# Kernel optimization log

Measured on AMD Instinct MI355X. Metric: run time of the kernel, lower is better.

The kernel has to match this reference:

```python
import jax, jax.numpy as jnp
from jax import lax
import numpy as np

RADIUS = 0.3
NSAMPLES = 32
SPATIAL_STRIDE = 32
TKS = 3
TSTRIDE = 2
DIM = 512
DEPTH = 4
HEADS = 8
DIM_HEAD = 64
MLP_DIM = 1024
NUM_CLASSES = 30
B, T, N = 4, 24, 4096


def setup_inputs():
    key = jax.random.key(0)
    ks = jax.random.split(key, 16)
    def w(k, shape, fan_in):
        return jax.random.normal(k, shape, jnp.float32) / np.float32(np.sqrt(fan_in))
    return {
        "xyzs": jax.random.uniform(ks[0], (B, T, N, 3), jnp.float32),
        "old_features": jax.random.normal(ks[1], (B, T, 2, N), jnp.float32),
        "conv_d_w": w(ks[2], (DIM, 4), 4),
        "conv_f_w": w(ks[3], (DIM, 2), 2),
        "pos_w": w(ks[4], (DIM, 4), 4),
        "pos_b": jnp.zeros((DIM,), jnp.float32),
        "contr_w": w(ks[5], (DIM, 4), 4),
        "contr_b": jnp.zeros((DIM,), jnp.float32),
        "ln1_s": jnp.ones((DEPTH, DIM), jnp.float32),
        "ln1_b": jnp.zeros((DEPTH, DIM), jnp.float32),
        "qkv_w": w(ks[6], (DEPTH, 3 * HEADS * DIM_HEAD, DIM), DIM),
        "out_w": w(ks[7], (DEPTH, DIM, HEADS * DIM_HEAD), HEADS * DIM_HEAD),
        "out_b": jnp.zeros((DEPTH, DIM), jnp.float32),
        "ln2_s": jnp.ones((DEPTH, DIM), jnp.float32),
        "ln2_b": jnp.zeros((DEPTH, DIM), jnp.float32),
        "ff1_w": w(ks[8], (DEPTH, MLP_DIM, DIM), DIM),
        "ff1_b": jnp.zeros((DEPTH, MLP_DIM), jnp.float32),
        "ff2_w": w(ks[9], (DEPTH, DIM, MLP_DIM), MLP_DIM),
        "ff2_b": jnp.zeros((DEPTH, DIM), jnp.float32),
        "head_ln_s": jnp.ones((DIM,), jnp.float32),
        "head_ln_b": jnp.zeros((DIM,), jnp.float32),
        "head1_w": w(ks[10], (MLP_DIM, DIM), DIM),
        "head1_b": jnp.zeros((MLP_DIM,), jnp.float32),
        "head2_w": w(ks[11], (NUM_CLASSES, MLP_DIM), MLP_DIM),
        "head2_b": jnp.zeros((NUM_CLASSES,), jnp.float32),
    }


def _fps(xyz, npoint):
    # furthest point sampling, pointnet2 semantics (start at index 0)
    n = xyz.shape[0]
    def body(carry, _):
        dist, last = carry
        d = jnp.sum((xyz - xyz[last]) ** 2, axis=-1)
        dist = jnp.minimum(dist, d)
        nxt = jnp.argmax(dist).astype(jnp.int32)
        return (dist, nxt), nxt
    init = (jnp.full((n,), 1e10, xyz.dtype), jnp.int32(0))
    _, idxs = lax.scan(body, init, None, length=npoint - 1)
    return jnp.concatenate([jnp.zeros((1,), jnp.int32), idxs])


def _ball_query(anchor, neighbor):
    # anchor [M,3], neighbor [N,3] -> [M,NSAMPLES] int32; first-k-in-radius, pad with first hit
    n = neighbor.shape[0]
    d2 = jnp.sum((anchor[:, None, :] - neighbor[None, :, :]) ** 2, axis=-1)
    pos = jnp.where(d2 < RADIUS * RADIUS, jnp.arange(n, dtype=jnp.int32), n)
    idx = -lax.top_k(-pos, NSAMPLES)[0]          # k smallest scan positions
    idx = jnp.where(idx == n, idx[:, :1], idx)   # pad with first found index
    return jnp.where(idx == n, 0, idx)           # nothing in radius -> 0


def _group(pts, idx):
    # pts [B,To,N,C], idx [B,To,M,K] -> [B,To,M,K,C]
    b, to, m, k = idx.shape
    g = jnp.take_along_axis(pts, idx.reshape(b, to, m * k)[..., None], axis=2)
    return g.reshape(b, to, m, k, pts.shape[-1])


def _p4dconv(xyzs, feats, conv_d_w, conv_f_w):
    b, t, n, _ = xyzs.shape
    m = n // SPATIAL_STRIDE
    rad = TKS // 2
    # temporal replicate padding [1,0]
    xyzs_p = jnp.concatenate([xyzs[:, :1], xyzs], axis=1)                             # [B,T+1,N,3]
    feats_p = jnp.concatenate([feats[:, :1], feats], axis=1).transpose(0, 1, 3, 2)    # [B,T+1,N,2]
    t_idx = np.arange(rad, t + 1 - rad, TSTRIDE)                                      # anchor frames (static)
    anchors = xyzs_p[:, t_idx]                                                        # [B,To,N,3]
    fps_idx = jax.vmap(jax.vmap(lambda x: _fps(x, m)))(anchors)                       # [B,To,M]
    anchor_xyz = jnp.take_along_axis(anchors, fps_idx[..., None], axis=2)             # [B,To,M,3]
    pooled = None
    for o in range(-rad, rad + 1):  # temporal kernel (small, structural)
        nb_xyz = xyzs_p[:, t_idx + o]
        nb_feat = feats_p[:, t_idx + o]
        idx = jax.vmap(jax.vmap(_ball_query))(anchor_xyz, nb_xyz)                     # [B,To,M,K]
        disp = _group(nb_xyz, idx) - anchor_xyz[:, :, :, None, :]                     # [B,To,M,K,3]
        disp4 = jnp.concatenate([disp, jnp.full(disp.shape[:-1] + (1,), float(o), disp.dtype)], axis=-1)
        d_emb = jnp.einsum('btmkc,dc->btmkd', disp4, conv_d_w)
        f_emb = jnp.einsum('btmkc,dc->btmkd', _group(nb_feat, idx), conv_f_w)
        feat = jnp.max(f_emb * d_emb, axis=3)                                          # spatial max-pool [B,To,M,D]
        pooled = feat if pooled is None else jnp.maximum(pooled, feat)                 # temporal max-pool
    return anchor_xyz, pooled


def _ln(x, s, b):
    mu = jnp.mean(x, axis=-1, keepdims=True)
    var = jnp.mean((x - mu) ** 2, axis=-1, keepdims=True)
    return (x - mu) / jnp.sqrt(var + 1e-5) * s + b


def reference(xyzs, old_features, conv_d_w, conv_f_w, pos_w, pos_b, contr_w, contr_b,
              ln1_s, ln1_b, qkv_w, out_w, out_b, ln2_s, ln2_b, ff1_w, ff1_b, ff2_w, ff2_b,
              head_ln_s, head_ln_b, head1_w, head1_b, head2_w, head2_b):
    new_xyz, feat = _p4dconv(xyzs, old_features, conv_d_w, conv_f_w)   # [B,To,M,3], [B,To,M,D]
    b, to, m, _ = new_xyz.shape
    tvals = jnp.arange(1, to + 1, dtype=new_xyz.dtype)
    xyzt = jnp.concatenate([new_xyz, jnp.broadcast_to(tvals[None, :, None, None], (b, to, m, 1))], axis=-1)
    xyzts = xyzt.reshape(b, to * m, 4)
    features = feat.reshape(b, to * m, DIM)
    pos = xyzts @ pos_w.T + pos_b                    # Conv1d(4,dim,k=1) == pointwise linear
    contrastive = xyzts @ contr_w.T + contr_b        # Linear(4,dim) on raw [x,y,z,t] tokens
    x = jax.nn.relu(pos + features)
    scale = DIM_HEAD ** -0.5
    for l in range(DEPTH):
        h = _ln(x, ln1_s[l], ln1_b[l])
        qkv = h @ qkv_w[l].T
        q, k, v = jnp.split(qkv, 3, axis=-1)
        q = q.reshape(b, -1, HEADS, DIM_HEAD)
        k = k.reshape(b, -1, HEADS, DIM_HEAD)
        v = v.reshape(b, -1, HEADS, DIM_HEAD)
        att = jax.nn.softmax(jnp.einsum('bihd,bjhd->bhij', q, k) * scale, axis=-1)
        o = jnp.einsum('bhij,bjhd->bihd', att, v).reshape(b, -1, HEADS * DIM_HEAD)
        x = x + o @ out_w[l].T + out_b[l]
        h = _ln(x, ln2_s[l], ln2_b[l])
        x = x + jax.nn.gelu(h @ ff1_w[l].T + ff1_b[l], approximate=False) @ ff2_w[l].T + ff2_b[l]
    pooled = jnp.max(x, axis=1)
    h = _ln(pooled, head_ln_s, head_ln_b)
    logits = jax.nn.gelu(h @ head1_w.T + head1_b, approximate=False) @ head2_w.T + head2_b
    return logits, contrastive, features
```

## Files before the change

### kernel.cpp

```cpp
#include <hip/hip_runtime.h>
#include <math.h>

#define BN_  4
#define TT   24
#define NN   4096
#define TO   12
#define MM   128
#define LL   (TO*MM)
#define BL   (BN_*LL)
#define DM   512
#define NH   8
#define DH   64
#define MLPD 1024
#define NC   30

#define OUT_LOGITS 0
#define OUT_CONTR  (BN_*NC)
#define OUT_FEATS  (OUT_CONTR + BL*DM)

#define NWQ   3145728
#define NWO   1048576
#define NWF1  2097152
#define NWF2  2097152
#define WQOFF   0
#define WOOFF   (NWQ)
#define WF1OFF  (NWQ+NWO)
#define WF2OFF  (NWQ+NWO+NWF1)
#define WTOT    (NWQ+NWO+NWF1+NWF2)

typedef __attribute__((ext_vector_type(8))) short s16x8;
typedef __attribute__((ext_vector_type(4))) float f32x4;
#define MFMA(a,b,c) __builtin_amdgcn_mfma_f32_16x16x32_bf16(a,b,c,0,0,0)

__device__ __forceinline__ void split_bf16(float a, short &h, short &l) {
  unsigned u = __float_as_uint(a);
  h = (short)(u >> 16);
  float ah = __uint_as_float(u & 0xffff0000u);
  float al = a - ah;
  l = (short)(__float_as_uint(al) >> 16);
}

__device__ __forceinline__ float d2_3(float ax, float ay, float az,
                                      float bx, float by, float bz) {
#pragma clang fp contract(off)
  float dx = ax - bx, dy = ay - by, dz = az - bz;
  float dx2 = dx * dx, dy2 = dy * dy, dz2 = dz * dz;
  return (dx2 + dy2) + dz2;
}

__device__ __forceinline__ float gelu_f(float v) {
  return 0.5f * v * (1.0f + erff(v * 0.70710678118654752440f));
}

__global__ __launch_bounds__(256) void splitw_kernel(
    const float* __restrict__ qkv_w, const float* __restrict__ out_w,
    const float* __restrict__ ff1_w, const float* __restrict__ ff2_w,
    short* __restrict__ wh, short* __restrict__ wl) {
  int i = blockIdx.x * 256 + threadIdx.x;
  const float* src; int off;
  if (i < WOOFF)        { src = qkv_w; off = i; }
  else if (i < WF1OFF)  { src = out_w; off = i - WOOFF; }
  else if (i < WF2OFF)  { src = ff1_w; off = i - WF1OFF; }
  else                  { src = ff2_w; off = i - WF2OFF; }
  float v = src[off];
  short h, l; split_bf16(v, h, l);
  wh[i] = h; wl[i] = l;
}

__global__ __launch_bounds__(256) void fps_kernel(const float* __restrict__ xyzs,
                                                  float* __restrict__ anchor) {
  __shared__ float sx[NN], sy[NN], sz[NN];
  __shared__ unsigned long long skey[2][4];
  int blk = blockIdx.x;
  int b = blk / TO, ti = blk - b * TO;
  const float* src = xyzs + ((size_t)(b * TT + 2 * ti)) * NN * 3;
  int tid = threadIdx.x;
  float dist[16], px[16], py[16], pz[16];
#pragma unroll
  for (int s = 0; s < 16; ++s) {
    int p = tid + s * 256;
    px[s] = src[p * 3 + 0]; py[s] = src[p * 3 + 1]; pz[s] = src[p * 3 + 2];
    sx[p] = px[s]; sy[p] = py[s]; sz[p] = pz[s];
    dist[s] = 1e10f;
  }
  __syncthreads();
  float lx = sx[0], ly = sy[0], lz = sz[0];
  float* aout = anchor + (size_t)blk * MM * 3;
  if (tid == 0) { aout[0] = lx; aout[1] = ly; aout[2] = lz; }
  for (int j = 1; j < MM; ++j) {
    unsigned long long best = 0;
#pragma unroll
    for (int s = 0; s < 16; ++s) {
      float d2 = d2_3(px[s], py[s], pz[s], lx, ly, lz);
      float dn = fminf(dist[s], d2);
      dist[s] = dn;
      unsigned long long key = ((unsigned long long)__float_as_uint(dn) << 12)
                               | (unsigned)(4095 - (tid + s * 256));
      best = key > best ? key : best;
    }
#pragma unroll
    for (int m = 1; m < 64; m <<= 1) {
      unsigned long long o = __shfl_xor(best, m, 64);
      best = o > best ? o : best;
    }
    if ((tid & 63) == 0) skey[j & 1][tid >> 6] = best;
    __syncthreads();
    unsigned long long b0 = skey[j & 1][0], b1 = skey[j & 1][1];
    unsigned long long b2 = skey[j & 1][2], b3 = skey[j & 1][3];
    unsigned long long bb = b0 > b1 ? b0 : b1;
    unsigned long long cc = b2 > b3 ? b2 : b3;
    bb = bb > cc ? bb : cc;
    int bi = 4095 - (int)(bb & 0xFFFull);
    lx = sx[bi]; ly = sy[bi]; lz = sz[bi];
    if (tid == 0) { aout[j * 3 + 0] = lx; aout[j * 3 + 1] = ly; aout[j * 3 + 2] = lz; }
  }
}

__global__ __launch_bounds__(64) void ballconv_kernel(
    const float* __restrict__ xyzs, const float* __restrict__ oldf,
    const float* __restrict__ anchor,
    const float* __restrict__ wdw, const float* __restrict__ wfw,
    float* __restrict__ dout) {
  __shared__ int   sidx[32];
  __shared__ float sdisp[32][4];
  __shared__ float sfeat[32][2];
  int blk = blockIdx.x;
  int b = blk / (TO * MM);
  int rem = blk - b * (TO * MM);
  int ti = rem / MM;
  int lane = threadIdx.x;
  const float* ap = anchor + (size_t)blk * 3;
  float ax = ap[0], ay = ap[1], az = ap[2];
  int d0 = lane * 8;
  float4 wd[8]; float2 wf[8];
#pragma unroll
  for (int jd = 0; jd < 8; ++jd) {
    wd[jd] = *(const float4*)(wdw + (d0 + jd) * 4);
    wf[jd] = *(const float2*)(wfw + (d0 + jd) * 2);
  }
  float fmx[8];
#pragma unroll
  for (int jd = 0; jd < 8; ++jd) fmx[jd] = -INFINITY;

  for (int o = -1; o <= 1; ++o) {
    int tp = 1 + 2 * ti + o;
    int orig = (tp == 0) ? 0 : tp - 1;
    const float* nx = xyzs + ((size_t)(b * TT + orig)) * NN * 3;
    const float* nf = oldf + ((size_t)(b * TT + orig)) * 2 * NN;
    int cnt = 0;
    for (int base = 0; base < NN && cnt < 32; base += 64) {
      int p = base + lane;
      float d2 = d2_3(ax, ay, az, nx[p * 3], nx[p * 3 + 1], nx[p * 3 + 2]);
      bool in = d2 < 0.09f;
      unsigned long long mask = __ballot(in);
      int pos = __popcll(mask & ((1ull << lane) - 1ull));
      if (in && (cnt + pos) < 32) sidx[cnt + pos] = p;
      cnt += __popcll(mask);
    }
    __syncthreads();
    int used = cnt < 32 ? cnt : 32;
    if (lane < 32 && lane >= used) sidx[lane] = (used > 0) ? sidx[0] : 0;
    __syncthreads();
    if (lane < 32) {
      int p = sidx[lane];
      sdisp[lane][0] = nx[p * 3 + 0] - ax;
      sdisp[lane][1] = nx[p * 3 + 1] - ay;
      sdisp[lane][2] = nx[p * 3 + 2] - az;
      sdisp[lane][3] = (float)o;
      sfeat[lane][0] = nf[p];
      sfeat[lane][1] = nf[NN + p];
    }
    __syncthreads();
    for (int k = 0; k < 32; ++k) {
      float p0 = sdisp[k][0], p1 = sdisp[k][1], p2 = sdisp[k][2], p3 = sdisp[k][3];
      float f0 = sfeat[k][0], f1 = sfeat[k][1];
#pragma unroll
      for (int jd = 0; jd < 8; ++jd) {
        float de = wd[jd].x * p0 + wd[jd].y * p1 + wd[jd].z * p2 + wd[jd].w * p3;
        float fe = wf[jd].x * f0 + wf[jd].y * f1;
        fmx[jd] = fmaxf(fmx[jd], fe * de);
      }
    }
    __syncthreads();
  }
  float* fout = dout + OUT_FEATS + (size_t)blk * DM + d0;
#pragma unroll
  for (int jd = 0; jd < 8; jd += 4)
    *(float4*)(fout + jd) = make_float4(fmx[jd], fmx[jd + 1], fmx[jd + 2], fmx[jd + 3]);
}

__global__ __launch_bounds__(256) void posx_kernel(
    const float* __restrict__ anchor,
    const float* __restrict__ pw, const float* __restrict__ pb,
    const float* __restrict__ cw, const float* __restrict__ cb,
    float* __restrict__ dout, float* __restrict__ x) {
  int idx = blockIdx.x * 256 + threadIdx.x;
  int bl = idx >> 9, d = idx & 511;
  int ti = (bl % LL) / MM;
  const float* ap = anchor + (size_t)bl * 3;
  float c0 = ap[0], c1 = ap[1], c2 = ap[2], c3 = (float)(ti + 1);
  float4 pwv = *(const float4*)(pw + d * 4);
  float4 cwv = *(const float4*)(cw + d * 4);
  float pos = pwv.x * c0 + pwv.y * c1 + pwv.z * c2 + pwv.w * c3 + pb[d];
  float con = cwv.x * c0 + cwv.y * c1 + cwv.z * c2 + cwv.w * c3 + cb[d];
  dout[OUT_CONTR + (size_t)idx] = con;
  float v = pos + dout[OUT_FEATS + (size_t)idx];
  x[idx] = v > 0.0f ? v : 0.0f;
}

__global__ __launch_bounds__(64) void ln_split_kernel(
    const float* __restrict__ x, const float* __restrict__ gs,
    const float* __restrict__ gb, short* __restrict__ oh, short* __restrict__ ol) {
  int row = blockIdx.x, lane = threadIdx.x;
  const float* xr = x + (size_t)row * DM + lane * 8;
  float4 v0 = *(const float4*)xr;
  float4 v1 = *(const float4*)(xr + 4);
  float v[8] = {v0.x, v0.y, v0.z, v0.w, v1.x, v1.y, v1.z, v1.w};
  float s = 0.f;
#pragma unroll
  for (int j = 0; j < 8; ++j) s += v[j];
  for (int m = 1; m < 64; m <<= 1) s += __shfl_xor(s, m, 64);
  float mu = s * (1.0f / DM);
  float d[8], ss = 0.f;
#pragma unroll
  for (int j = 0; j < 8; ++j) { d[j] = v[j] - mu; ss += d[j] * d[j]; }
  for (int m = 1; m < 64; m <<= 1) ss += __shfl_xor(ss, m, 64);
  float rs = 1.0f / sqrtf(ss * (1.0f / DM) + 1e-5f);
  const float* gsr = gs + lane * 8;
  const float* gbr = gb + lane * 8;
  s16x8 hv, lv;
#pragma unroll
  for (int j = 0; j < 8; ++j) {
    float f = d[j] * rs * gsr[j] + gbr[j];
    short h, l; split_bf16(f, h, l);
    hv[j] = h; lv[j] = l;
  }
  *(s16x8*)(oh + (size_t)row * DM + lane * 8) = hv;
  *(s16x8*)(ol + (size_t)row * DM + lane * 8) = lv;
}

__global__ __launch_bounds__(64) void ln_kernel(
    const float* __restrict__ x, const float* __restrict__ gs,
    const float* __restrict__ gb, float* __restrict__ out) {
  int row = blockIdx.x, lane = threadIdx.x;
  const float* xr = x + (size_t)row * DM + lane * 8;
  float4 v0 = *(const float4*)xr;
  float4 v1 = *(const float4*)(xr + 4);
  float v[8] = {v0.x, v0.y, v0.z, v0.w, v1.x, v1.y, v1.z, v1.w};
  float s = 0.f;
#pragma unroll
  for (int j = 0; j < 8; ++j) s += v[j];
  for (int m = 1; m < 64; m <<= 1) s += __shfl_xor(s, m, 64);
  float mu = s * (1.0f / DM);
  float d[8], ss = 0.f;
#pragma unroll
  for (int j = 0; j < 8; ++j) { d[j] = v[j] - mu; ss += d[j] * d[j]; }
  for (int m = 1; m < 64; m <<= 1) ss += __shfl_xor(ss, m, 64);
  float rs = 1.0f / sqrtf(ss * (1.0f / DM) + 1e-5f);
  const float* gsr = gs + lane * 8;
  const float* gbr = gb + lane * 8;
  float* orow = out + (size_t)row * DM + lane * 8;
  float r[8];
#pragma unroll
  for (int j = 0; j < 8; ++j) r[j] = d[j] * rs * gsr[j] + gbr[j];
  *(float4*)orow       = make_float4(r[0], r[1], r[2], r[3]);
  *(float4*)(orow + 4) = make_float4(r[4], r[5], r[6], r[7]);
}

template <int EPI>
__global__ __launch_bounds__(256) void mgemm_kernel(
    const short* __restrict__ Ah, const short* __restrict__ Al,
    const short* __restrict__ Wh, const short* __restrict__ Wl,
    const float* __restrict__ bias, const float* __restrict__ res,
    float* __restrict__ Cf, short* __restrict__ Ch, short* __restrict__ Cl,
    short* __restrict__ vTh, short* __restrict__ vTl,
    int M, int N, int K) {
  __shared__ short As[2][128 * 40];
  __shared__ short Ws[2][128 * 40];
  int tid = threadIdx.x;
  int lane = tid & 63, w = tid >> 6;
  int wr = w >> 1, wc = w & 1;
  int row0 = blockIdx.y * 128, col0 = blockIdx.x * 128;
  int srow = tid >> 1, skc = (tid & 1) * 16;
  const short* Ahp = Ah + (size_t)(row0 + srow) * K + skc;
  const short* Alp = Al + (size_t)(row0 + srow) * K + skc;
  const short* Whp = Wh + (size_t)(col0 + srow) * K + skc;
  const short* Wlp = Wl + (size_t)(col0 + srow) * K + skc;
  int fr = lane & 15, fk = (lane >> 4) * 8;
  f32x4 acc[16];
#pragma unroll
  for (int i = 0; i < 16; ++i) acc[i] = (f32x4){0.f, 0.f, 0.f, 0.f};
  s16x8 rA0 = *(const s16x8*)(Ahp);
  s16x8 rA1 = *(const s16x8*)(Ahp + 8);
  s16x8 rA2 = *(const s16x8*)(Alp);
  s16x8 rA3 = *(const s16x8*)(Alp + 8);
  s16x8 rW0 = *(const s16x8*)(Whp);
  s16x8 rW1 = *(const s16x8*)(Whp + 8);
  s16x8 rW2 = *(const s16x8*)(Wlp);
  s16x8 rW3 = *(const s16x8*)(Wlp + 8);
  for (int ks = 0; ks < K; ks += 32) {
    __syncthreads();
    *(s16x8*)&As[0][srow * 40 + skc]     = rA0;
    *(s16x8*)&As[0][srow * 40 + skc + 8] = rA1;
    *(s16x8*)&As[1][srow * 40 + skc]     = rA2;
    *(s16x8*)&As[1][srow * 40 + skc + 8] = rA3;
    *(s16x8*)&Ws[0][srow * 40 + skc]     = rW0;
    *(s16x8*)&Ws[0][srow * 40 + skc + 8] = rW1;
    *(s16x8*)&Ws[1][srow * 40 + skc]     = rW2;
    *(s16x8*)&Ws[1][srow * 40 + skc + 8] = rW3;
    __syncthreads();
    if (ks + 32 < K) {
      rA0 = *(const s16x8*)(Ahp + ks + 32);
      rA1 = *(const s16x8*)(Ahp + ks + 40);
      rA2 = *(const s16x8*)(Alp + ks + 32);
      rA3 = *(const s16x8*)(Alp + ks + 40);
      rW0 = *(const s16x8*)(Whp + ks + 32);
      rW1 = *(const s16x8*)(Whp + ks + 40);
      rW2 = *(const s16x8*)(Wlp + ks + 32);
      rW3 = *(const s16x8*)(Wlp + ks + 40);
    }
    s16x8 bh_[4], bl_[4];
#pragma unroll
    for (int t = 0; t < 4; ++t) {
      bh_[t] = *(const s16x8*)&Ws[0][(wc * 64 + t * 16 + fr) * 40 + fk];
      bl_[t] = *(const s16x8*)&Ws[1][(wc * 64 + t * 16 + fr) * 40 + fk];
    }
#pragma unroll
    for (int a = 0; a < 4; ++a) {
      s16x8 ah_ = *(const s16x8*)&As[0][(wr * 64 + a * 16 + fr) * 40 + fk];
      s16x8 al_ = *(const s16x8*)&As[1][(wr * 64 + a * 16 + fr) * 40 + fk];
#pragma unroll
      for (int t = 0; t < 4; ++t) {
        f32x4 c = acc[a * 4 + t];
        c = MFMA(ah_, bh_[t], c);
        c = MFMA(ah_, bl_[t], c);
        c = MFMA(al_, bh_[t], c);
        acc[a * 4 + t] = c;
      }
    }
  }
  int fq = lane >> 4;
  if (EPI == 1) {
    int bidx = row0 / LL;
    int j0 = row0 - bidx * LL + wr * 64;
    float qscale = (col0 < 512) ? 0.125f : 1.0f;
#pragma unroll
    for (int a = 0; a < 4; ++a) {
#pragma unroll
      for (int t = 0; t < 4; ++t) {
        int c = col0 + wc * 64 + t * 16 + fr;
        f32x4 v = acc[a * 4 + t];
        if (col0 < 1024) {
#pragma unroll
          for (int r = 0; r < 4; ++r) {
            int row = row0 + wr * 64 + a * 16 + fq * 4 + r;
            size_t off = (size_t)row * 1024 + c;
            short h, l; split_bf16(v[r] * qscale, h, l);
            Ch[off] = h; Cl[off] = l;
          }
        } else {
          int vcol = c - 1024;
          size_t vidx = ((size_t)(bidx * 8 + (vcol >> 6)) * 64 + (vcol & 63)) * LL
                        + j0 + a * 16 + fq * 4;
          short4 hv, lv;
          short h, l;
          split_bf16(v[0], h, l); hv.x = h; lv.x = l;
          split_bf16(v[1], h, l); hv.y = h; lv.y = l;
          split_bf16(v[2], h, l); hv.z = h; lv.z = l;
          split_bf16(v[3], h, l); hv.w = h; lv.w = l;
          *(short4*)(vTh + vidx) = hv;
          *(short4*)(vTl + vidx) = lv;
        }
      }
    }
  } else {
#pragma unroll
    for (int a = 0; a < 4; ++a) {
#pragma unroll
      for (int t = 0; t < 4; ++t) {
#pragma unroll
        for (int r = 0; r < 4; ++r) {
          int row = row0 + wr * 64 + a * 16 + fq * 4 + r;
          int c   = col0 + wc * 64 + t * 16 + fr;
          size_t off = (size_t)row * N + c;
          float v = acc[a * 4 + t][r] + bias[c];
          if (EPI == 2) {
            v = gelu_f(v);
            short h, l; split_bf16(v, h, l);
            Ch[off] = h; Cl[off] = l;
          } else {
            Cf[off] = v + res[off];
          }
        }
      }
    }
  }
}

__global__ __launch_bounds__(256) void mattn_kernel(
    const short* __restrict__ qkh, const short* __restrict__ qkl,
    const short* __restrict__ vTh, const short* __restrict__ vTl,
    short* __restrict__ oh, short* __restrict__ ol) {
  __shared__ short Ks[2][64 * 72];
  __shared__ short Vs[2][64 * 72];
  __shared__ short Ps[2][64 * 72];
  int it = blockIdx.x, bh = blockIdx.y;
  int b = bh >> 3, h = bh & 7;
  int tid = threadIdx.x, lane = tid & 63, w = tid >> 6;
  int fr = lane & 15, fq = lane >> 4, fk = fq * 8;
  size_t rowbase = (size_t)b * LL;
  s16x8 qfh[2], qfl[2];
  {
    size_t qoff = (size_t)(rowbase + it * 64 + w * 16 + fr) * 1024 + h * DH;
    qfh[0] = *(const s16x8*)(qkh + qoff + fk);
    qfh[1] = *(const s16x8*)(qkh + qoff + 32 + fk);
    qfl[0] = *(const s16x8*)(qkl + qoff + fk);
    qfl[1] = *(const s16x8*)(qkl + qoff + 32 + fk);
  }
  const short* vbh = vTh + (size_t)(b * 8 + h) * 64 * LL;
  const short* vbl = vTl + (size_t)(b * 8 + h) * 64 * LL;
  float m_i[4], l_i[4];
  f32x4 oac[4];
#pragma unroll
  for (int r = 0; r < 4; ++r) { m_i[r] = -INFINITY; l_i[r] = 0.f; }
#pragma unroll
  for (int t = 0; t < 4; ++t) oac[t] = (f32x4){0.f, 0.f, 0.f, 0.f};
  int kjr = tid >> 2, kc0 = (tid & 3) * 16;
  for (int jt = 0; jt < LL / 64; ++jt) {
    size_t kbase = (size_t)(rowbase + jt * 64 + kjr) * 1024 + 512 + h * DH + kc0;
    s16x8 k0 = *(const s16x8*)(qkh + kbase);
    s16x8 k1 = *(const s16x8*)(qkh + kbase + 8);
    s16x8 k2 = *(const s16x8*)(qkl + kbase);
    s16x8 k3 = *(const s16x8*)(qkl + kbase + 8);
    size_t vgb = (size_t)kjr * LL + jt * 64 + kc0;
    s16x8 v0 = *(const s16x8*)(vbh + vgb);
    s16x8 v1 = *(const s16x8*)(vbh + vgb + 8);
    s16x8 v2 = *(const s16x8*)(vbl + vgb);
    s16x8 v3 = *(const s16x8*)(vbl + vgb + 8);
    __syncthreads();
    *(s16x8*)&Ks[0][kjr * 72 + kc0]     = k0;
    *(s16x8*)&Ks[0][kjr * 72 + kc0 + 8] = k1;
    *(s16x8*)&Ks[1][kjr * 72 + kc0]     = k2;
    *(s16x8*)&Ks[1][kjr * 72 + kc0 + 8] = k3;
    *(s16x8*)&Vs[0][kjr * 72 + kc0]     = v0;
    *(s16x8*)&Vs[0][kjr * 72 + kc0 + 8] = v1;
    *(s16x8*)&Vs[1][kjr * 72 + kc0]     = v2;
    *(s16x8*)&Vs[1][kjr * 72 + kc0 + 8] = v3;
    __syncthreads();
    f32x4 s[4];
#pragma unroll
    for (int t = 0; t < 4; ++t) s[t] = (f32x4){0.f, 0.f, 0.f, 0.f};
#pragma unroll
    for (int ks = 0; ks < 2; ++ks) {
#pragma unroll
      for (int t = 0; t < 4; ++t) {
        s16x8 kh_ = *(const s16x8*)&Ks[0][(t * 16 + fr) * 72 + ks * 32 + fk];
        s16x8 kl_ = *(const s16x8*)&Ks[1][(t * 16 + fr) * 72 + ks * 32 + fk];
        s[t] = MFMA(qfh[ks], kh_, s[t]);
        s[t] = MFMA(qfh[ks], kl_, s[t]);
        s[t] = MFMA(qfl[ks], kh_, s[t]);
      }
    }
#pragma unroll
    for (int r = 0; r < 4; ++r) {
      float s0 = s[0][r], s1 = s[1][r], s2 = s[2][r], s3 = s[3][r];
      float mr = fmaxf(fmaxf(s0, s1), fmaxf(s2, s3));
      mr = fmaxf(mr, __shfl_xor(mr, 1, 64));
      mr = fmaxf(mr, __shfl_xor(mr, 2, 64));
      mr = fmaxf(mr, __shfl_xor(mr, 4, 64));
      mr = fmaxf(mr, __shfl_xor(mr, 8, 64));
      float mn = fmaxf(m_i[r], mr);
      float al = expf(m_i[r] - mn);
      float p0 = expf(s0 - mn), p1 = expf(s1 - mn);
      float p2 = expf(s2 - mn), p3 = expf(s3 - mn);
      float ps = p0 + p1 + p2 + p3;
      ps += __shfl_xor(ps, 1, 64); ps += __shfl_xor(ps, 2, 64);
      ps += __shfl_xor(ps, 4, 64); ps += __shfl_xor(ps, 8, 64);
      l_i[r] = l_i[r] * al + ps;
      m_i[r] = mn;
      oac[0][r] *= al; oac[1][r] *= al; oac[2][r] *= al; oac[3][r] *= al;
      int prow = (w * 16 + fq * 4 + r) * 72;
      short hh_, ll_;
      split_bf16(p0, hh_, ll_); Ps[0][prow + fr]      = hh_; Ps[1][prow + fr]      = ll_;
      split_bf16(p1, hh_, ll_); Ps[0][prow + 16 + fr] = hh_; Ps[1][prow + 16 + fr] = ll_;
      split_bf16(p2, hh_, ll_); Ps[0][prow + 32 + fr] = hh_; Ps[1][prow + 32 + fr] = ll_;
      split_bf16(p3, hh_, ll_); Ps[0][prow + 48 + fr] = hh_; Ps[1][prow + 48 + fr] = ll_;
    }
#pragma unroll
    for (int ks = 0; ks < 2; ++ks) {
      s16x8 ph_ = *(const s16x8*)&Ps[0][(w * 16 + fr) * 72 + ks * 32 + fk];
      s16x8 pl_ = *(const s16x8*)&Ps[1][(w * 16 + fr) * 72 + ks * 32 + fk];
#pragma unroll
      for (int t = 0; t < 4; ++t) {
        s16x8 vh_ = *(const s16x8*)&Vs[0][(t * 16 + fr) * 72 + ks * 32 + fk];
        s16x8 vl_ = *(const s16x8*)&Vs[1][(t * 16 + fr) * 72 + ks * 32 + fk];
        oac[t] = MFMA(ph_, vh_, oac[t]);
        oac[t] = MFMA(ph_, vl_, oac[t]);
        oac[t] = MFMA(pl_, vh_, oac[t]);
      }
    }
  }
#pragma unroll
  for (int r = 0; r < 4; ++r) {
    float inv = 1.0f / l_i[r];
    size_t row = rowbase + it * 64 + w * 16 + fq * 4 + r;
#pragma unroll
    for (int t = 0; t < 4; ++t) {
      float v = oac[t][r] * inv;
      short hh_, ll_; split_bf16(v, hh_, ll_);
      size_t off = row * DM + h * DH + t * 16 + fr;
      oh[off] = hh_; ol[off] = ll_;
    }
  }
}

__global__ __launch_bounds__(256) void poolmax1_kernel(const float* __restrict__ x,
                                                       float* __restrict__ partial) {
  int ch = blockIdx.x, b = blockIdx.y, tid = threadIdx.x;
  const float* p = x + ((size_t)b * LL + ch * 128) * DM;
  float m0 = -INFINITY, m1 = -INFINITY;
#pragma unroll 4
  for (int l = 0; l < 128; ++l) {
    m0 = fmaxf(m0, p[(size_t)l * DM + tid]);
    m1 = fmaxf(m1, p[(size_t)l * DM + tid + 256]);
  }
  partial[(size_t)(b * TO + ch) * DM + tid] = m0;
  partial[(size_t)(b * TO + ch) * DM + tid + 256] = m1;
}

__global__ __launch_bounds__(256) void poolmax2_kernel(const float* __restrict__ partial,
                                                       float* __restrict__ pooled) {
  int idx = blockIdx.x * 256 + threadIdx.x;
  int b = idx >> 9, d = idx & 511;
  float m = -INFINITY;
#pragma unroll
  for (int c = 0; c < TO; ++c) m = fmaxf(m, partial[(size_t)(b * TO + c) * DM + d]);
  pooled[idx] = m;
}

__global__ __launch_bounds__(256) void head1_kernel(const float* __restrict__ lnp,
                                                    const float* __restrict__ w,
                                                    const float* __restrict__ bb,
                                                    float* __restrict__ hid) {
  int idx = blockIdx.x * 256 + threadIdx.x;
  int b = idx >> 10, n = idx & 1023;
  const float* xr = lnp + (size_t)b * DM;
  const float* wr = w + (size_t)n * DM;
  float s = 0.f;
  for (int k = 0; k < DM; k += 4) {
    float4 xv = *(const float4*)(xr + k);
    float4 wv = *(const float4*)(wr + k);
    s += xv.x * wv.x + xv.y * wv.y + xv.z * wv.z + xv.w * wv.w;
  }
  hid[idx] = gelu_f(s + bb[n]);
}

__global__ __launch_bounds__(128) void head2_kernel(const float* __restrict__ hid,
                                                    const float* __restrict__ w,
                                                    const float* __restrict__ bb,
                                                    float* __restrict__ dout) {
  int t = threadIdx.x;
  if (t < BN_ * NC) {
    int b = t / NC, n = t - b * NC;
    const float* xr = hid + (size_t)b * MLPD;
    const float* wr = w + (size_t)n * MLPD;
    float s = 0.f;
    for (int k = 0; k < MLPD; k += 4) {
      float4 xv = *(const float4*)(xr + k);
      float4 wv = *(const float4*)(wr + k);
      s += xv.x * wv.x + xv.y * wv.y + xv.z * wv.z + xv.w * wv.w;
    }
    dout[OUT_LOGITS + t] = s + bb[n];
  }
}

extern "C" void kernel_launch(void* const* d_in, const int* in_sizes, int n_in,
                              void* d_out, int out_size, void* d_ws, size_t ws_size,
                              hipStream_t stream) {
  (void)in_sizes; (void)n_in; (void)out_size; (void)ws_size;
  const float* xyzs     = (const float*)d_in[0];
  const float* oldf     = (const float*)d_in[1];
  const float* conv_d_w = (const float*)d_in[2];
  const float* conv_f_w = (const float*)d_in[3];
  const float* pos_w    = (const float*)d_in[4];
  const float* pos_b    = (const float*)d_in[5];
  const float* contr_w  = (const float*)d_in[6];
  const float* contr_b  = (const float*)d_in[7];
  const float* ln1_s    = (const float*)d_in[8];
  const float* ln1_b    = (const float*)d_in[9];
  const float* qkv_w    = (const float*)d_in[10];
  const float* out_w    = (const float*)d_in[11];
  const float* out_b    = (const float*)d_in[12];
  const float* ln2_s    = (const float*)d_in[13];
  const float* ln2_b    = (const float*)d_in[14];
  const float* ff1_w    = (const float*)d_in[15];
  const float* ff1_b    = (const float*)d_in[16];
  const float* ff2_w    = (const float*)d_in[17];
  const float* ff2_b    = (const float*)d_in[18];
  const float* hl_s     = (const float*)d_in[19];
  const float* hl_b     = (const float*)d_in[20];
  const float* h1_w     = (const float*)d_in[21];
  const float* h1_b     = (const float*)d_in[22];
  const float* h2_w     = (const float*)d_in[23];
  const float* h2_b     = (const float*)d_in[24];
  float* dout = (float*)d_out;
  char* base = (char*)d_ws;
  auto alloc = [&](size_t bytes) { char* p = base; base += (bytes + 255) & ~(size_t)255; return p; };

  float* anchor = (float*)alloc((size_t)BN_ * TO * MM * 3 * 4);
  float* x      = (float*)alloc((size_t)BL * DM * 4);
  short* qkvh   = (short*)alloc((size_t)BL * 1024 * 2);
  short* qkvl   = (short*)alloc((size_t)BL * 1024 * 2);
  short* vTh    = (short*)alloc((size_t)BN_ * NH * DH * LL * 2);
  short* vTl    = (short*)alloc((size_t)BN_ * NH * DH * LL * 2);
  short* atnh   = (short*)alloc((size_t)BL * DM * 2);
  short* atnl   = (short*)alloc((size_t)BL * DM * 2);
  short* hh     = (short*)alloc((size_t)BL * DM * 2);
  short* hl     = (short*)alloc((size_t)BL * DM * 2);
  short* wsh    = (short*)alloc((size_t)WTOT * 2);
  short* wsl    = (short*)alloc((size_t)WTOT * 2);
  float* partial= (float*)alloc((size_t)BN_ * TO * DM * 4);
  float* pooled = (float*)alloc((size_t)BN_ * DM * 4);
  float* lnp    = (float*)alloc((size_t)BN_ * DM * 4);
  float* hid    = (float*)alloc((size_t)BN_ * MLPD * 4);
  short* fh = qkvh;
  short* fl = qkvl;

  splitw_kernel<<<WTOT / 256, 256, 0, stream>>>(qkv_w, out_w, ff1_w, ff2_w, wsh, wsl);
  fps_kernel<<<BN_ * TO, 256, 0, stream>>>(xyzs, anchor);
  ballconv_kernel<<<BN_ * TO * MM, 64, 0, stream>>>(xyzs, oldf, anchor, conv_d_w, conv_f_w, dout);
  posx_kernel<<<(BL * DM) / 256, 256, 0, stream>>>(anchor, pos_w, pos_b, contr_w, contr_b, dout, x);

  for (int l = 0; l < 4; ++l) {
    ln_split_kernel<<<BL, 64, 0, stream>>>(x, ln1_s + l * DM, ln1_b + l * DM, hh, hl);
    mgemm_kernel<1><<<dim3(1536 / 128, BL / 128), 256, 0, stream>>>(
        hh, hl, wsh + WQOFF + (size_t)l * 786432, wsl + WQOFF + (size_t)l * 786432,
        nullptr, nullptr, nullptr, qkvh, qkvl, vTh, vTl, BL, 1536, DM);
    mattn_kernel<<<dim3(LL / 64, BN_ * NH), 256, 0, stream>>>(qkvh, qkvl, vTh, vTl, atnh, atnl);
    mgemm_kernel<3><<<dim3(DM / 128, BL / 128), 256, 0, stream>>>(
        atnh, atnl, wsh + WOOFF + (size_t)l * 262144, wsl + WOOFF + (size_t)l * 262144,
        out_b + l * DM, x, x, nullptr, nullptr, nullptr, nullptr, BL, DM, DM);
    ln_split_kernel<<<BL, 64, 0, stream>>>(x, ln2_s + l * DM, ln2_b + l * DM, hh, hl);
    mgemm_kernel<2><<<dim3(MLPD / 128, BL / 128), 256, 0, stream>>>(
        hh, hl, wsh + WF1OFF + (size_t)l * 524288, wsl + WF1OFF + (size_t)l * 524288,
        ff1_b + l * MLPD, nullptr, nullptr, fh, fl, nullptr, nullptr, BL, MLPD, DM);
    mgemm_kernel<3><<<dim3(DM / 128, BL / 128), 256, 0, stream>>>(
        fh, fl, wsh + WF2OFF + (size_t)l * 524288, wsl + WF2OFF + (size_t)l * 524288,
        ff2_b + l * DM, x, x, nullptr, nullptr, nullptr, nullptr, BL, DM, MLPD);
  }

  poolmax1_kernel<<<dim3(TO, BN_), 256, 0, stream>>>(x, partial);
  poolmax2_kernel<<<(BN_ * DM) / 256, 256, 0, stream>>>(partial, pooled);
  ln_kernel<<<BN_, 64, 0, stream>>>(pooled, hl_s, hl_b, lnp);
  head1_kernel<<<(BN_ * MLPD) / 256, 256, 0, stream>>>(lnp, h1_w, h1_b, hid);
  head2_kernel<<<1, 128, 0, stream>>>(hid, h2_w, h2_b, dout);
}
```

Measured before the change: 1.639 ms.

## Double attention query tile to 128 rows with 512-thread blocks

The attention kernel now processes 128 query rows per block using 8 wavefronts instead of 64 rows with 4, so each K/V tile staged in shared memory is reused by twice as many queries. This halves the global K/V traffic per query. The launch is flattened to a 1D grid with head/batch in the low bits, so blocks sharing the same K/V run adjacently and can share L2. The cost is fewer blocks (384 instead of 768), larger blocks, and more shared memory for P, which may reduce occupancy.

New measurement: 1.591 ms. -2.9%, faster.

```diff
diff --git a/kernel.cpp b/kernel.cpp
--- a/kernel.cpp
+++ b/kernel.cpp
@@ -397,21 +397,22 @@
   }
 }
 
-__global__ __launch_bounds__(256) void mattn_kernel(
+__global__ __launch_bounds__(512) void mattn_kernel(
     const short* __restrict__ qkh, const short* __restrict__ qkl,
     const short* __restrict__ vTh, const short* __restrict__ vTl,
     short* __restrict__ oh, short* __restrict__ ol) {
   __shared__ short Ks[2][64 * 72];
   __shared__ short Vs[2][64 * 72];
-  __shared__ short Ps[2][64 * 72];
-  int it = blockIdx.x, bh = blockIdx.y;
+  __shared__ short Ps[2][128 * 72];
+  int n = blockIdx.x;
+  int bh = n & 31, it = n >> 5;
   int b = bh >> 3, h = bh & 7;
   int tid = threadIdx.x, lane = tid & 63, w = tid >> 6;
   int fr = lane & 15, fq = lane >> 4, fk = fq * 8;
   size_t rowbase = (size_t)b * LL;
   s16x8 qfh[2], qfl[2];
   {
-    size_t qoff = (size_t)(rowbase + it * 64 + w * 16 + fr) * 1024 + h * DH;
+    size_t qoff = (size_t)(rowbase + it * 128 + w * 16 + fr) * 1024 + h * DH;
     qfh[0] = *(const s16x8*)(qkh + qoff + fk);
     qfh[1] = *(const s16x8*)(qkh + qoff + 32 + fk);
     qfl[0] = *(const s16x8*)(qkl + qoff + fk);
@@ -425,27 +426,19 @@
   for (int r = 0; r < 4; ++r) { m_i[r] = -INFINITY; l_i[r] = 0.f; }
 #pragma unroll
   for (int t = 0; t < 4; ++t) oac[t] = (f32x4){0.f, 0.f, 0.f, 0.f};
-  int kjr = tid >> 2, kc0 = (tid & 3) * 16;
+  int sr = tid >> 3, sc = (tid & 7) * 8;
   for (int jt = 0; jt < LL / 64; ++jt) {
-    size_t kbase = (size_t)(rowbase + jt * 64 + kjr) * 1024 + 512 + h * DH + kc0;
+    size_t kbase = (size_t)(rowbase + jt * 64 + sr) * 1024 + 512 + h * DH + sc;
     s16x8 k0 = *(const s16x8*)(qkh + kbase);
-    s16x8 k1 = *(const s16x8*)(qkh + kbase + 8);
-    s16x8 k2 = *(const s16x8*)(qkl + kbase);
-    s16x8 k3 = *(const s16x8*)(qkl + kbase + 8);
-    size_t vgb = (size_t)kjr * LL + jt * 64 + kc0;
+    s16x8 k1 = *(const s16x8*)(qkl + kbase);
+    size_t vgb = (size_t)sr * LL + jt * 64 + sc;
     s16x8 v0 = *(const s16x8*)(vbh + vgb);
-    s16x8 v1 = *(const s16x8*)(vbh + vgb + 8);
-    s16x8 v2 = *(const s16x8*)(vbl + vgb);
-    s16x8 v3 = *(const s16x8*)(vbl + vgb + 8);
-    __syncthreads();
-    *(s16x8*)&Ks[0][kjr * 72 + kc0]     = k0;
-    *(s16x8*)&Ks[0][kjr * 72 + kc0 + 8] = k1;
-    *(s16x8*)&Ks[1][kjr * 72 + kc0]     = k2;
-    *(s16x8*)&Ks[1][kjr * 72 + kc0 + 8] = k3;
-    *(s16x8*)&Vs[0][kjr * 72 + kc0]     = v0;
-    *(s16x8*)&Vs[0][kjr * 72 + kc0 + 8] = v1;
-    *(s16x8*)&Vs[1][kjr * 72 + kc0]     = v2;
-    *(s16x8*)&Vs[1][kjr * 72 + kc0 + 8] = v3;
+    s16x8 v1 = *(const s16x8*)(vbl + vgb);
+    __syncthreads();
+    *(s16x8*)&Ks[0][sr * 72 + sc] = k0;
+    *(s16x8*)&Ks[1][sr * 72 + sc] = k1;
+    *(s16x8*)&Vs[0][sr * 72 + sc] = v0;
+    *(s16x8*)&Vs[1][sr * 72 + sc] = v1;
     __syncthreads();
     f32x4 s[4];
 #pragma unroll
@@ -503,7 +496,7 @@
 #pragma unroll
   for (int r = 0; r < 4; ++r) {
     float inv = 1.0f / l_i[r];
-    size_t row = rowbase + it * 64 + w * 16 + fq * 4 + r;
+    size_t row = rowbase + it * 128 + w * 16 + fq * 4 + r;
 #pragma unroll
     for (int t = 0; t < 4; ++t) {
       float v = oac[t][r] * inv;
@@ -636,7 +629,7 @@
     mgemm_kernel<1><<<dim3(1536 / 128, BL / 128), 256, 0, stream>>>(
         hh, hl, wsh + WQOFF + (size_t)l * 786432, wsl + WQOFF + (size_t)l * 786432,
         nullptr, nullptr, nullptr, qkvh, qkvl, vTh, vTl, BL, 1536, DM);
-    mattn_kernel<<<dim3(LL / 64, BN_ * NH), 256, 0, stream>>>(qkvh, qkvl, vTh, vTl, atnh, atnl);
+    mattn_kernel<<<dim3((LL / 128) * 32), 512, 0, stream>>>(qkvh, qkvl, vTh, vTl, atnh, atnl);
     mgemm_kernel<3><<<dim3(DM / 128, BL / 128), 256, 0, stream>>>(
         atnh, atnl, wsh + WOOFF + (size_t)l * 262144, wsl + WOOFF + (size_t)l * 262144,
         out_b + l * DM, x, x, nullptr, nullptr, nullptr, nullptr, BL, DM, DM);
```
